# Performance work log

Hardware: AMD Instinct MI355X
Metric: run time of the kernel (lower is better)

Reference implementation:

```python
import jax, jax.numpy as jnp
import numpy as np
import math

PI = math.pi
PATCH_SIZE = 32
NUM_BINS = 36
EPS = 1e-8


def setup_inputs() -> dict:
    key = jax.random.key(0)
    patch = jax.random.normal(key, (65536, 1, PATCH_SIZE, PATCH_SIZE), dtype=jnp.float32)
    return {"patch": patch}


def reference(patch):
    B = patch.shape[0]
    dt = patch.dtype
    # kornia SpatialGradient('sobel', 1): L1-normalized sobel kernels, replicate padding
    kx = jnp.array([[-1.0, 0.0, 1.0], [-2.0, 0.0, 2.0], [-1.0, 0.0, 1.0]], dtype=dt) / 8.0
    ky = kx.T
    kernel = jnp.stack([kx, ky])[:, None]  # [2,1,3,3] OIHW
    padded = jnp.pad(patch, ((0, 0), (0, 0), (1, 1), (1, 1)), mode="edge")
    grads = jax.lax.conv_general_dilated(
        padded, kernel, window_strides=(1, 1), padding="VALID",
        dimension_numbers=("NCHW", "OIHW", "NCHW"))  # [B,2,H,W]
    gx, gy = grads[:, 0], grads[:, 1]
    mag = jnp.sqrt(gx * gx + gy * gy + EPS)
    ori = jnp.arctan2(gy, gx + EPS) + 2.0 * PI
    o_big = float(NUM_BINS) * (ori + PI) / (2.0 * PI)
    bo0 = jnp.floor(o_big)
    wo1 = o_big - bo0
    b0 = (bo0 % NUM_BINS).astype(jnp.int32)
    b1 = (b0 + 1) % NUM_BINS
    w0 = (1.0 - wo1) * mag
    w1 = wo1 * mag
    npix = PATCH_SIZE * PATCH_SIZE
    # soft histogram via scatter-add; adaptive_avg_pool2d(1,1) == mean over pixels
    def histo(b0f, b1f, w0f, w1f):
        return jnp.zeros(NUM_BINS, dtype=dt).at[b0f].add(w0f).at[b1f].add(w1f)
    hist = jax.vmap(histo)(b0.reshape(B, -1), b1.reshape(B, -1),
                           w0.reshape(B, -1), w1.reshape(B, -1)) / npix
    # circular conv1d with fixed kernel [0.33, 0.34, 0.33]
    sm = 0.33 * jnp.roll(hist, 1, axis=-1) + 0.34 * hist + 0.33 * jnp.roll(hist, -1, axis=-1)
    indices = jnp.argmax(sm, axis=-1)
    angle = -(2.0 * PI * indices.astype(dt) / float(NUM_BINS) - PI)
    return angle
```

## Files before the change

### kernel.cpp

```cpp
#include <hip/hip_runtime.h>
#include <math.h>

#pragma clang fp contract(off)

#define NBINS 36
#define PS 32

__device__ __forceinline__ float atan2_np(float fy, float fx)
{
    const double aT0  =  3.33333333333329318027e-01;
    const double aT1  = -1.99999999998764832476e-01;
    const double aT2  =  1.42857142725034663711e-01;
    const double aT3  = -1.11111104054623557880e-01;
    const double aT4  =  9.09088713343650656196e-02;
    const double aT5  = -7.69187620504482999495e-02;
    const double aT6  =  6.66107313738753120669e-02;
    const double aT7  = -5.83357013379057348645e-02;
    const double aT8  =  4.97687799461593236017e-02;
    const double aT9  = -3.65315727442169155270e-02;
    const double aT10 =  1.62858201153657823623e-02;

    float axf = fabsf(fx), ayf = fabsf(fy);
    float uf = fmaxf(axf, ayf), vf = fminf(axf, ayf);
    bool g1 = vf >= 0.41421356f * uf;

    double u = (double)uf, v = (double)vf;
    double c      = g1 ? 1.0 : 0.0;
    double atc_hi = g1 ? 7.85398163397448278999e-01 : 0.0;
    double atc_lo = g1 ? 3.06161699786838301793e-17 : 0.0;

    double num = fma(-c, u, v);
    double den = fma(c, v, u);

    double r0 = __builtin_amdgcn_rcp(den);
    r0 = fma(fma(-den, r0, 1.0), r0, r0);
    r0 = fma(fma(-den, r0, 1.0), r0, r0);
    double q0 = num * r0;
    double xq = fma(fma(-den, q0, num), r0, q0);

    double z = xq * xq;
    double w = z * z;
    double s1_ = z * fma(w, fma(w, fma(w, fma(w, fma(w, aT10, aT8), aT6), aT4), aT2), aT0);
    double s2_ = w * fma(w, fma(w, fma(w, fma(w, aT9, aT7), aT5), aT3), aT1);
    double p   = xq * (s1_ + s2_);
    double res = atc_hi - ((p - atc_lo) - xq);

    double res2 = (1.57079632679489655800e+00 - res) + 6.12323399573676603587e-17;
    res = (ayf > axf) ? res2 : res;
    double res3 = (3.14159265358979311600e+00 - res) + 1.22464679914735317723e-16;
    res = (fx < 0.0f) ? res3 : res;
    res = copysign(res, (double)fy);
    return (float)res;
}

__global__ __launch_bounds__(256)
void patch_orient_kernel(const float* __restrict__ patches, float* __restrict__ out)
{
    __shared__ __align__(16) float tile[PS][PS];
    __shared__ __align__(16) unsigned bm[NBINS][36];
    __shared__ __align__(16) unsigned pref32[NBINS][16];
    __shared__ unsigned short cnt[NBINS];
    __shared__ unsigned short start[NBINS];
    __shared__ __align__(16) float s0[1024];
    __shared__ __align__(16) float s1[1024];
    __shared__ float hsm[NBINS];

    const int t = threadIdx.x;
    const int b = blockIdx.x;
    const float* p = patches + (size_t)b * (PS * PS);

    #pragma unroll
    for (int i = t; i < NBINS * 32; i += 256) bm[i >> 5][i & 31] = 0u;

    ((float4*)tile)[t] = ((const float4*)p)[t];
    __syncthreads();

    const int row = t >> 3;
    const int cb  = (t & 7) << 2;
    const int rm  = (row == 0)  ? 0  : row - 1;
    const int rp  = (row == 31) ? 31 : row + 1;

    float win[3][6];
    {
        const int cl = (cb == 0)  ? 0  : cb - 1;
        const int cr = (cb == 28) ? 31 : cb + 4;
        const int rows[3] = {rm, row, rp};
        #pragma unroll
        for (int r = 0; r < 3; ++r) {
            float4 v = *((const float4*)&tile[rows[r]][cb]);
            win[r][0] = tile[rows[r]][cl];
            win[r][1] = v.x; win[r][2] = v.y; win[r][3] = v.z; win[r][4] = v.w;
            win[r][5] = tile[rows[r]][cr];
        }
    }

    const float TWO_PI = 6.2831853071795864769f;
    const float PI_F   = 3.14159265358979323846f;

    float w0r[4], w1r[4];
    int   binr[4];

    #pragma unroll
    for (int i = 0; i < 4; ++i) {
        float A = win[0][i], B = win[0][i + 1], C = win[0][i + 2];
        float D = win[1][i],                    F = win[1][i + 2];
        float G = win[2][i], H = win[2][i + 1], I = win[2][i + 2];

        float gx = -0.125f * A;
        gx += 0.125f  * C;
        gx += -0.25f  * D;
        gx += 0.25f   * F;
        gx += -0.125f * G;
        gx += 0.125f  * I;

        float gy = -0.125f * A;
        gy += -0.25f  * B;
        gy += -0.125f * C;
        gy += 0.125f  * G;
        gy += 0.25f   * H;
        gy += 0.125f  * I;

        float m1 = gx * gx;
        float m2 = gy * gy;
        float s  = m1 + m2;
        s = s + 1e-8f;
        float mag = sqrtf(s);

        float gxe = gx + 1e-8f;
        float at  = atan2_np(gy, gxe);
        float ori = at + TWO_PI;
        float obig = (36.0f * (ori + PI_F)) / TWO_PI;
        float bo0  = floorf(obig);
        float wo1  = obig - bo0;

        int bi0 = (int)bo0 - 36;
        if (bi0 < 0)   bi0 += 36;
        if (bi0 >= 36) bi0 -= 36;

        w0r[i]  = (1.0f - wo1) * mag;
        w1r[i]  = wo1 * mag;
        binr[i] = bi0;
        atomicOr(&bm[bi0][row], 1u << (cb + i));
    }
    __syncthreads();

    if (t < 64) {
        unsigned run = 0;
        if (t < NBINS) {
            const uint4* bw = (const uint4*)&bm[t][0];
            uint4* pw = (uint4*)&pref32[t][0];
            #pragma unroll
            for (int k = 0; k < 4; ++k) {
                uint4 wa = bw[2 * k], wb = bw[2 * k + 1];
                unsigned p0 = run;
                unsigned p1 = p0 + __popc(wa.x);
                unsigned p2 = p1 + __popc(wa.y);
                unsigned p3 = p2 + __popc(wa.z);
                unsigned p4 = p3 + __popc(wa.w);
                unsigned p5 = p4 + __popc(wb.x);
                unsigned p6 = p5 + __popc(wb.y);
                unsigned p7 = p6 + __popc(wb.z);
                run = p7 + __popc(wb.w);
                uint4 pk;
                pk.x = p0 | (p1 << 16);
                pk.y = p2 | (p3 << 16);
                pk.z = p4 | (p5 << 16);
                pk.w = p6 | (p7 << 16);
                pw[k] = pk;
            }
            cnt[t] = (unsigned short)run;
        }
        unsigned v = run;
        #pragma unroll
        for (int d = 1; d < 64; d <<= 1) {
            unsigned o = (unsigned)__shfl_up((int)v, d);
            if (t >= d) v += o;
        }
        if (t < NBINS) start[t] = (unsigned short)(v - run);
    }
    __syncthreads();

    #pragma unroll
    for (int i = 0; i < 4; ++i) {
        const int bi = binr[i];
        unsigned pv = pref32[bi][row >> 1];
        pv = (row & 1) ? (pv >> 16) : (pv & 0xffffu);
        const unsigned lowmask = (1u << (cb + i)) - 1u;
        const int pos = (int)start[bi] + (int)pv
                      + __popc(bm[bi][row] & lowmask);
        s0[pos] = w0r[i];
        s1[pos] = w1r[i];
    }
    __syncthreads();

    if (t < NBINS) {
        float acc = 0.0f;
        {
            int i = start[t], en = i + cnt[t];
            int lim = (i + 3) & ~3; if (lim > en) lim = en;
            for (; i < lim; ++i) acc += s0[i];
            for (; i + 4 <= en; i += 4) {
                float4 v4 = *((const float4*)&s0[i]);
                acc += v4.x; acc += v4.y; acc += v4.z; acc += v4.w;
            }
            for (; i < en; ++i) acc += s0[i];
        }
        {
            int t2 = (t == 0) ? NBINS - 1 : t - 1;
            int i = start[t2], en = i + cnt[t2];
            int lim = (i + 3) & ~3; if (lim > en) lim = en;
            for (; i < lim; ++i) acc += s1[i];
            for (; i + 4 <= en; i += 4) {
                float4 v4 = *((const float4*)&s1[i]);
                acc += v4.x; acc += v4.y; acc += v4.z; acc += v4.w;
            }
            for (; i < en; ++i) acc += s1[i];
        }
        hsm[t] = acc * (1.0f / 1024.0f);
    }
    __syncthreads();

    if (t < 64) {
        float val = -1.0f;
        int   idx = t;
        if (t < NBINS) {
            int im_ = (t == 0)         ? NBINS - 1 : t - 1;
            int ip_ = (t == NBINS - 1) ? 0         : t + 1;
            float q0 = 0.33f * hsm[im_];
            float q1 = 0.34f * hsm[t];
            float q2 = 0.33f * hsm[ip_];
            val = (q0 + q1) + q2;
        }
        #pragma unroll
        for (int d = 1; d < 64; d <<= 1) {
            float ov = __shfl_xor(val, d);
            int   oi = __shfl_xor(idx, d);
            if (ov > val || (ov == val && oi < idx)) { val = ov; idx = oi; }
        }
        if (t == 0) {
            float t1 = TWO_PI * (float)idx;
            float t2 = t1 / 36.0f;
            float t3 = t2 - PI_F;
            out[b] = -t3;
        }
    }
}

extern "C" void kernel_launch(void* const* d_in, const int* in_sizes, int n_in,
                              void* d_out, int out_size, void* d_ws, size_t ws_size,
                              hipStream_t stream) {
    const float* patch = (const float*)d_in[0];
    float* out = (float*)d_out;
    const int B = in_sizes[0] / (PS * PS);
    patch_orient_kernel<<<B, 256, 0, stream>>>(patch, out);
}
```

Before: 550.1 us.

## Use DPP lane shifts for halo, transpose bin bitmaps, replace divide with reciprocal FMA

The left and right halo columns of the Sobel window now come from neighbouring lanes through DPP row shifts instead of extra shared-memory loads. The bin bitmap is transposed to [row][bin] and the per-bin prefix becomes a serial loop over rows writing 16-bit prefixes. The division by two pi becomes a reciprocal multiply with one Newton-style FMA correction. The histogram reduction switches from float4 loads to scalar pairs, and the q2 line gains a strange term multiplied by zero. These changes risk small numerical differences and a longer serial prefix loop, and the zero-term edit looks like a bug.

```diff
diff --git a/kernel.cpp b/kernel.cpp
--- a/kernel.cpp
+++ b/kernel.cpp
@@ -53,12 +53,23 @@
     return (float)res;
 }
 
+__device__ __forceinline__ float dpp_prev(float x) {
+    int i = __builtin_bit_cast(int, x);
+    int r = __builtin_amdgcn_update_dpp(i, i, 0x111, 0xf, 0xf, false);
+    return __builtin_bit_cast(float, r);
+}
+__device__ __forceinline__ float dpp_next(float x) {
+    int i = __builtin_bit_cast(int, x);
+    int r = __builtin_amdgcn_update_dpp(i, i, 0x101, 0xf, 0xf, false);
+    return __builtin_bit_cast(float, r);
+}
+
 __global__ __launch_bounds__(256)
 void patch_orient_kernel(const float* __restrict__ patches, float* __restrict__ out)
 {
     __shared__ __align__(16) float tile[PS][PS];
-    __shared__ __align__(16) unsigned bm[NBINS][36];
-    __shared__ __align__(16) unsigned pref32[NBINS][16];
+    __shared__ unsigned bm[PS][NBINS];
+    __shared__ unsigned short pref[PS][NBINS];
     __shared__ unsigned short cnt[NBINS];
     __shared__ unsigned short start[NBINS];
     __shared__ __align__(16) float s0[1024];
@@ -70,7 +81,7 @@
     const float* p = patches + (size_t)b * (PS * PS);
 
     #pragma unroll
-    for (int i = t; i < NBINS * 32; i += 256) bm[i >> 5][i & 31] = 0u;
+    for (int i = t; i < PS * NBINS; i += 256) ((unsigned*)bm)[i] = 0u;
 
     ((float4*)tile)[t] = ((const float4*)p)[t];
     __syncthreads();
@@ -82,20 +93,21 @@
 
     float win[3][6];
     {
-        const int cl = (cb == 0)  ? 0  : cb - 1;
-        const int cr = (cb == 28) ? 31 : cb + 4;
         const int rows[3] = {rm, row, rp};
         #pragma unroll
         for (int r = 0; r < 3; ++r) {
             float4 v = *((const float4*)&tile[rows[r]][cb]);
-            win[r][0] = tile[rows[r]][cl];
+            float lf = dpp_prev(v.w);
+            float rt = dpp_next(v.x);
+            win[r][0] = (cb == 0)  ? v.x : lf;
             win[r][1] = v.x; win[r][2] = v.y; win[r][3] = v.z; win[r][4] = v.w;
-            win[r][5] = tile[rows[r]][cr];
+            win[r][5] = (cb == 28) ? v.w : rt;
         }
     }
 
     const float TWO_PI = 6.2831853071795864769f;
     const float PI_F   = 3.14159265358979323846f;
+    const float INV2PI = 0.15915493667125701904f;
 
     float w0r[4], w1r[4];
     int   binr[4];
@@ -129,7 +141,9 @@
         float gxe = gx + 1e-8f;
         float at  = atan2_np(gy, gxe);
         float ori = at + TWO_PI;
-        float obig = (36.0f * (ori + PI_F)) / TWO_PI;
+        float xn  = 36.0f * (ori + PI_F);
+        float q1m = xn * INV2PI;
+        float obig = fmaf(fmaf(-TWO_PI, q1m, xn), INV2PI, q1m);
         float bo0  = floorf(obig);
         float wo1  = obig - bo0;
 
@@ -140,33 +154,17 @@
         w0r[i]  = (1.0f - wo1) * mag;
         w1r[i]  = wo1 * mag;
         binr[i] = bi0;
-        atomicOr(&bm[bi0][row], 1u << (cb + i));
+        atomicOr(&bm[row][bi0], 1u << (cb + i));
     }
     __syncthreads();
 
     if (t < 64) {
         unsigned run = 0;
         if (t < NBINS) {
-            const uint4* bw = (const uint4*)&bm[t][0];
-            uint4* pw = (uint4*)&pref32[t][0];
-            #pragma unroll
-            for (int k = 0; k < 4; ++k) {
-                uint4 wa = bw[2 * k], wb = bw[2 * k + 1];
-                unsigned p0 = run;
-                unsigned p1 = p0 + __popc(wa.x);
-                unsigned p2 = p1 + __popc(wa.y);
-                unsigned p3 = p2 + __popc(wa.z);
-                unsigned p4 = p3 + __popc(wa.w);
-                unsigned p5 = p4 + __popc(wb.x);
-                unsigned p6 = p5 + __popc(wb.y);
-                unsigned p7 = p6 + __popc(wb.z);
-                run = p7 + __popc(wb.w);
-                uint4 pk;
-                pk.x = p0 | (p1 << 16);
-                pk.y = p2 | (p3 << 16);
-                pk.z = p4 | (p5 << 16);
-                pk.w = p6 | (p7 << 16);
-                pw[k] = pk;
+            #pragma unroll 1
+            for (int w = 0; w < PS; ++w) {
+                pref[w][t] = (unsigned short)run;
+                run += __popc(bm[w][t]);
             }
             cnt[t] = (unsigned short)run;
         }
@@ -183,11 +181,9 @@
     #pragma unroll
     for (int i = 0; i < 4; ++i) {
         const int bi = binr[i];
-        unsigned pv = pref32[bi][row >> 1];
-        pv = (row & 1) ? (pv >> 16) : (pv & 0xffffu);
         const unsigned lowmask = (1u << (cb + i)) - 1u;
-        const int pos = (int)start[bi] + (int)pv
-                      + __popc(bm[bi][row] & lowmask);
+        const int pos = (int)start[bi] + (int)pref[row][bi]
+                      + __popc(bm[row][bi] & lowmask);
         s0[pos] = w0r[i];
         s1[pos] = w1r[i];
     }
@@ -197,24 +193,14 @@
         float acc = 0.0f;
         {
             int i = start[t], en = i + cnt[t];
-            int lim = (i + 3) & ~3; if (lim > en) lim = en;
-            for (; i < lim; ++i) acc += s0[i];
-            for (; i + 4 <= en; i += 4) {
-                float4 v4 = *((const float4*)&s0[i]);
-                acc += v4.x; acc += v4.y; acc += v4.z; acc += v4.w;
-            }
-            for (; i < en; ++i) acc += s0[i];
+            for (; i + 1 < en; i += 2) { acc += s0[i]; acc += s0[i + 1]; }
+            if (i < en) acc += s0[i];
         }
         {
             int t2 = (t == 0) ? NBINS - 1 : t - 1;
             int i = start[t2], en = i + cnt[t2];
-            int lim = (i + 3) & ~3; if (lim > en) lim = en;
-            for (; i < lim; ++i) acc += s1[i];
-            for (; i + 4 <= en; i += 4) {
-                float4 v4 = *((const float4*)&s1[i]);
-                acc += v4.x; acc += v4.y; acc += v4.z; acc += v4.w;
-            }
-            for (; i < en; ++i) acc += s1[i];
+            for (; i + 1 < en; i += 2) { acc += s1[i]; acc += s1[i + 1]; }
+            if (i < en) acc += s1[i];
         }
         hsm[t] = acc * (1.0f / 1024.0f);
     }
@@ -228,7 +214,7 @@
             int ip_ = (t == NBINS - 1) ? 0         : t + 1;
             float q0 = 0.33f * hsm[im_];
             float q1 = 0.34f * hsm[t];
-            float q2 = 0.33f * hsm[ip_];
+            float q2 = 0.33f * hsm[t == NBINS - 1 ? 0 : t + 1] * 0.0f + 0.33f * hsm[ip_];
             val = (q0 + q1) + q2;
         }
         #pragma unroll
```

Result: faster. 522.8 us (-5.0%).
